# Performance work log

Measured on AMD Instinct MI355X. Metric: run time of the kernel, lower is better.

Reference implementation:

```python
import jax, jax.numpy as jnp
import numpy as np

NUM_CLASSES = 5
SMOOTH = 1e-5


def setup_inputs() -> dict:
    key = jax.random.key(0)
    k1, k2, k3 = jax.random.split(key, 3)
    B, C, X, Y, Z = 2, NUM_CLASSES, 128, 128, 128
    net_output = jax.random.normal(k1, (B, C, X, Y, Z), dtype=jnp.float32)
    target = jax.random.randint(k2, (B, 1, X, Y, Z), 0, C, dtype=jnp.int64)
    dist = jax.random.uniform(k3, (B, 1, X, Y, Z), dtype=jnp.float32)
    return {"net_output": net_output, "target": target, "dist": dist}


def reference(net_output, target, dist):
    # --- Distance-map penalized multi-class Dice ---
    p = jax.nn.softmax(net_output, axis=1)  # (B,C,X,Y,Z)
    gt = target[:, 0]  # (B,X,Y,Z)
    classes = jnp.arange(NUM_CLASSES)[None, :, None, None, None]
    y_onehot = (gt[:, None] == classes).astype(p.dtype)  # (B,C,X,Y,Z)
    # per-class, per-batch sums over spatial dims
    tp = jnp.sum(p * y_onehot * dist, axis=(2, 3, 4))  # (B,C), dist broadcasts over C
    denom = jnp.sum(p, axis=(2, 3, 4)) + jnp.sum(y_onehot, axis=(2, 3, 4))  # (B,C)
    dc = (2.0 * tp + SMOOTH) / (denom + SMOOTH)  # (B,C)
    # sum over classes of batch-mean, divided by num_classes == overall mean
    dpdc_loss = -jnp.mean(dc)
    # --- Cross entropy (mean over all voxels), target squeezed to class idx ---
    logp = jax.nn.log_softmax(net_output, axis=1)  # (B,C,X,Y,Z)
    nll = -jnp.take_along_axis(logp, target, axis=1)  # (B,1,X,Y,Z)
    ce_loss = jnp.mean(nll)
    # aggregate == 'sum', weight_ce = weight_dice = 1
    return ce_loss + dpdc_loss
```

## Files before the change

### kernel.cpp

```cpp
#include <hip/hip_runtime.h>

#define NC 5
#define NB 2
#define SPATIAL (128*128*128)
#define WTILE_VOX 256
#define BTILE_VOX 1024
#define NSTEPS (SPATIAL/BTILE_VOX)
#define GX 256
#define TPB (NSTEPS/GX)
#define SMOOTHF 1e-5f

#define WBUF 8192


__device__ __forceinline__ void async16(const void* g, void* l) {
    __builtin_amdgcn_global_load_lds(
        (const __attribute__((address_space(1))) void*)g,
        (__attribute__((address_space(3))) void*)l, 16, 0, 0);
}

__global__ __launch_bounds__(256) void dpdc_main(
    const float* __restrict__ net, const void* __restrict__ targ,
    const float* __restrict__ dist, float* __restrict__ slots)
{
    __shared__ __align__(16) char lds[2][4][WBUF];
    const int tid = threadIdx.x, wave = tid >> 6, lane = tid & 63;
    const int b = blockIdx.y;

    const unsigned long long tv = ((const unsigned long long*)targ)[lane];
    const int t64 = (__ballot(tv >= 5ull) == 0ull);

    const char* netb  = (const char*)net  + (size_t)b * NC * SPATIAL * 4;
    const char* distb = (const char*)dist + (size_t)b * SPATIAL * 4;
    const char* targb = (const char*)targ + (size_t)b * SPATIAL * (t64 ? 8 : 4);

    const size_t vb0 = (size_t)blockIdx.x * TPB * BTILE_VOX
                     + (size_t)wave * WTILE_VOX;

    auto stage = [&](int k, int bf) {
        char* base = &lds[bf][wave][0];
        const size_t vb = vb0 + (size_t)k * BTILE_VOX;
        const char* ns = netb + vb * 4 + lane * 16;
        #pragma unroll
        for (int c = 0; c < NC; ++c)
            async16(ns + (size_t)c * SPATIAL * 4, base + c * 1024 + lane * 16);
        async16(distb + vb * 4 + lane * 16, base + 5120 + lane * 16);
        if (t64) {
            const char* ts = targb + vb * 8 + lane * 16;
            async16(ts,        base + 6144 + lane * 16);
            async16(ts + 1024, base + 7168 + lane * 16);
        } else {
            const char* ts = targb + vb * 4 + lane * 16;
            async16(ts, base + 6144 + lane * 16);
            async16(ts, base + 7168 + lane * 16);
        }
    };

    float tp[NC], sp[NC];
    #pragma unroll
    for (int c = 0; c < NC; ++c) { tp[c] = 0.f; sp[c] = 0.f; }
    unsigned cntp = 0u;
    float nll = 0.f;

    stage(0, 0);

    #pragma unroll 1
    for (int k = 0; k < TPB; ++k) {
        if (k + 1 < TPB) {
            stage(k + 1, (k + 1) & 1);
            asm volatile("s_waitcnt vmcnt(8)" ::: "memory");
        } else {
            asm volatile("s_waitcnt vmcnt(0)" ::: "memory");
        }
        __builtin_amdgcn_sched_barrier(0);

        const char* base = &lds[k & 1][wave][0];
        float4 l[NC];
        #pragma unroll
        for (int c = 0; c < NC; ++c)
            l[c] = *(const float4*)(base + c * 1024 + lane * 16);
        float4 dd = *(const float4*)(base + 5120 + lane * 16);
        int tt[4];
        if (t64) {
            ulonglong2 a = *(const ulonglong2*)(base + 6144 + lane * 32);
            ulonglong2 q = *(const ulonglong2*)(base + 6144 + lane * 32 + 16);
            tt[0] = (int)a.x; tt[1] = (int)a.y;
            tt[2] = (int)q.x; tt[3] = (int)q.y;
        } else {
            int4 a = *(const int4*)(base + 6144 + lane * 16);
            tt[0] = a.x; tt[1] = a.y; tt[2] = a.z; tt[3] = a.w;
        }
        const float* dv = (const float*)&dd;
        #pragma unroll
        for (int j = 0; j < 4; ++j) {
            float lc[NC];
            #pragma unroll
            for (int c = 0; c < NC; ++c) lc[c] = ((const float*)&l[c])[j];
            float e[NC];
            float s = 0.f;
            #pragma unroll
            for (int c = 0; c < NC; ++c) { e[c] = __expf(lc[c]); s += e[c]; }
            float inv = 1.0f / s;
            int t = tt[j];
            float lsel = lc[4];
            #pragma unroll
            for (int c = 0; c < 4; ++c) lsel = (t == c) ? lc[c] : lsel;
            float pd = dv[j] * inv;
            #pragma unroll
            for (int c = 0; c < NC; ++c) {
                float p = e[c] * inv;
                sp[c] += p;
                tp[c] += (t == c) ? e[c] * pd : 0.f;
            }
            cntp += 1u << (6 * t);
            nll += __logf(s) - lsel;
        }
        asm volatile("s_waitcnt lgkmcnt(0)" ::: "memory");
        __builtin_amdgcn_sched_barrier(0);
    }

    __shared__ float red[4][16];
    float vals[16];
    #pragma unroll
    for (int c = 0; c < NC; ++c) {
        vals[c] = tp[c]; vals[5 + c] = sp[c];
        vals[10 + c] = (float)((cntp >> (6 * c)) & 63u);
    }
    vals[15] = nll;
    #pragma unroll
    for (int k = 0; k < 16; ++k) {
        float v = vals[k];
        #pragma unroll
        for (int off = 32; off > 0; off >>= 1) v += __shfl_down(v, off, 64);
        if (lane == 0) red[wave][k] = v;
    }
    __syncthreads();
    if (tid < 16) {
        float v = red[0][tid] + red[1][tid] + red[2][tid] + red[3][tid];
        slots[((size_t)b * GX + blockIdx.x) * 16 + tid] = v;
    }
}

__global__ __launch_bounds__(1024) void finalize(const float* __restrict__ slots,
                                                 float* __restrict__ out) {
    __shared__ float part[1024];
    __shared__ float tot[32];
    const int j = threadIdx.x;
    const int p = j & 31;
    const int b = p >> 4, k = p & 15;
    float s = 0.f;
    for (int slot = j >> 5; slot < GX; slot += 32)
        s += slots[((size_t)b * GX + slot) * 16 + k];
    part[j] = s;
    __syncthreads();
    if (j < 32) {
        float t = 0.f;
        #pragma unroll
        for (int m = 0; m < 32; ++m) t += part[j + 32 * m];
        tot[j] = t;
    }
    __syncthreads();
    if (j == 0) {
        float dcsum = 0.f;
        for (int bb = 0; bb < NB; ++bb)
            for (int c = 0; c < NC; ++c) {
                float tpv = tot[bb * 16 + c];
                float spv = tot[bb * 16 + 5 + c];
                float cv  = tot[bb * 16 + 10 + c];
                dcsum += (2.f * tpv + SMOOTHF) / (spv + cv + SMOOTHF);
            }
        float ce = (tot[15] + tot[31]) / (float)((size_t)NB * SPATIAL);
        out[0] = ce - dcsum / (float)(NB * NC);
    }
}

extern "C" void kernel_launch(void* const* d_in, const int* in_sizes, int n_in,
                              void* d_out, int out_size, void* d_ws, size_t ws_size,
                              hipStream_t stream) {
    const float* net  = (const float*)d_in[0];
    const void*  targ = d_in[1];
    const float* dist = (const float*)d_in[2];
    float* slots = (float*)d_ws;

    dim3 grid(GX, NB);
    dpdc_main<<<grid, 256, 0, stream>>>(net, targ, dist, slots);
    finalize<<<1, 1024, 0, stream>>>(slots, (float*)d_out);
}
```

Before: 32.43 us.

## Fuse finalize into main kernel via last-block atomic counter; template target width

Removes the separate finalize kernel launch: each block publishes its partial sums with atomics, bumps a global done counter, and the last block to arrive performs the final reduction and writes the loss. The target-width branch is also made a compile-time template, so the int32 path issues one target load per stage instead of a duplicated one and waits with a matching vmcnt. It relies on the workspace counter being zero or 0xAA-filled at start and being reset by the last block. Atomic reads in the tail add some latency to the final block.

New measurement: 33.21 us. 1.02x slower.

```diff
diff --git a/kernel.cpp b/kernel.cpp
--- a/kernel.cpp
+++ b/kernel.cpp
@@ -8,9 +8,10 @@
 #define NSTEPS (SPATIAL/BTILE_VOX)
 #define GX 256
 #define TPB (NSTEPS/GX)
+#define TOTAL_BLOCKS (GX*NB)
 #define SMOOTHF 1e-5f
-
 #define WBUF 8192
+
 
 
 __device__ __forceinline__ void async16(const void* g, void* l) {
@@ -19,24 +20,12 @@
         (__attribute__((address_space(3))) void*)l, 16, 0, 0);
 }
 
-__global__ __launch_bounds__(256) void dpdc_main(
-    const float* __restrict__ net, const void* __restrict__ targ,
-    const float* __restrict__ dist, float* __restrict__ slots)
+template<bool T64>
+__device__ __forceinline__ void pipeline(
+    const char* netb, const char* targb, const char* distb, size_t vb0,
+    int wave, int lane, char (*lds)[4][WBUF],
+    float* tp, float* sp, unsigned& cntp, float& nll)
 {
-    __shared__ __align__(16) char lds[2][4][WBUF];
-    const int tid = threadIdx.x, wave = tid >> 6, lane = tid & 63;
-    const int b = blockIdx.y;
-
-    const unsigned long long tv = ((const unsigned long long*)targ)[lane];
-    const int t64 = (__ballot(tv >= 5ull) == 0ull);
-
-    const char* netb  = (const char*)net  + (size_t)b * NC * SPATIAL * 4;
-    const char* distb = (const char*)dist + (size_t)b * SPATIAL * 4;
-    const char* targb = (const char*)targ + (size_t)b * SPATIAL * (t64 ? 8 : 4);
-
-    const size_t vb0 = (size_t)blockIdx.x * TPB * BTILE_VOX
-                     + (size_t)wave * WTILE_VOX;
-
     auto stage = [&](int k, int bf) {
         char* base = &lds[bf][wave][0];
         const size_t vb = vb0 + (size_t)k * BTILE_VOX;
@@ -45,22 +34,14 @@
         for (int c = 0; c < NC; ++c)
             async16(ns + (size_t)c * SPATIAL * 4, base + c * 1024 + lane * 16);
         async16(distb + vb * 4 + lane * 16, base + 5120 + lane * 16);
-        if (t64) {
+        if constexpr (T64) {
             const char* ts = targb + vb * 8 + lane * 16;
             async16(ts,        base + 6144 + lane * 16);
             async16(ts + 1024, base + 7168 + lane * 16);
         } else {
-            const char* ts = targb + vb * 4 + lane * 16;
-            async16(ts, base + 6144 + lane * 16);
-            async16(ts, base + 7168 + lane * 16);
+            async16(targb + vb * 4 + lane * 16, base + 6144 + lane * 16);
         }
     };
-
-    float tp[NC], sp[NC];
-    #pragma unroll
-    for (int c = 0; c < NC; ++c) { tp[c] = 0.f; sp[c] = 0.f; }
-    unsigned cntp = 0u;
-    float nll = 0.f;
 
     stage(0, 0);
 
@@ -68,7 +49,10 @@
     for (int k = 0; k < TPB; ++k) {
         if (k + 1 < TPB) {
             stage(k + 1, (k + 1) & 1);
-            asm volatile("s_waitcnt vmcnt(8)" ::: "memory");
+            if constexpr (T64)
+                asm volatile("s_waitcnt vmcnt(8)" ::: "memory");
+            else
+                asm volatile("s_waitcnt vmcnt(7)" ::: "memory");
         } else {
             asm volatile("s_waitcnt vmcnt(0)" ::: "memory");
         }
@@ -81,7 +65,7 @@
             l[c] = *(const float4*)(base + c * 1024 + lane * 16);
         float4 dd = *(const float4*)(base + 5120 + lane * 16);
         int tt[4];
-        if (t64) {
+        if constexpr (T64) {
             ulonglong2 a = *(const ulonglong2*)(base + 6144 + lane * 32);
             ulonglong2 q = *(const ulonglong2*)(base + 6144 + lane * 32 + 16);
             tt[0] = (int)a.x; tt[1] = (int)a.y;
@@ -118,6 +102,37 @@
         asm volatile("s_waitcnt lgkmcnt(0)" ::: "memory");
         __builtin_amdgcn_sched_barrier(0);
     }
+}
+
+__global__ __launch_bounds__(256) void dpdc_main(
+    const float* __restrict__ net, const void* __restrict__ targ,
+    const float* __restrict__ dist, float* __restrict__ slots,
+    unsigned* __restrict__ done, float* __restrict__ out)
+{
+    __shared__ __align__(16) char lds[2][4][WBUF];
+    const int tid = threadIdx.x, wave = tid >> 6, lane = tid & 63;
+    const int b = blockIdx.y;
+
+    const unsigned long long tv = ((const unsigned long long*)targ)[lane];
+    const int t64 = (__ballot(tv >= 5ull) == 0ull);
+
+    const char* netb  = (const char*)net  + (size_t)b * NC * SPATIAL * 4;
+    const char* distb = (const char*)dist + (size_t)b * SPATIAL * 4;
+    const char* targb = (const char*)targ + (size_t)b * SPATIAL * (t64 ? 8 : 4);
+
+    const size_t vb0 = (size_t)blockIdx.x * TPB * BTILE_VOX
+                     + (size_t)wave * WTILE_VOX;
+
+    float tp[NC], sp[NC];
+    #pragma unroll
+    for (int c = 0; c < NC; ++c) { tp[c] = 0.f; sp[c] = 0.f; }
+    unsigned cntp = 0u;
+    float nll = 0.f;
+
+    if (t64) pipeline<true >(netb, targb, distb, vb0, wave, lane, lds,
+                             tp, sp, cntp, nll);
+    else     pipeline<false>(netb, targb, distb, vb0, wave, lane, lds,
+                             tp, sp, cntp, nll);
 
     __shared__ float red[4][16];
     float vals[16];
@@ -135,38 +150,58 @@
         if (lane == 0) red[wave][k] = v;
     }
     __syncthreads();
+
+    const int slot = b * GX + blockIdx.x;
     if (tid < 16) {
         float v = red[0][tid] + red[1][tid] + red[2][tid] + red[3][tid];
-        slots[((size_t)b * GX + blockIdx.x) * 16 + tid] = v;
-    }
-}
-
-__global__ __launch_bounds__(1024) void finalize(const float* __restrict__ slots,
-                                                 float* __restrict__ out) {
-    __shared__ float part[1024];
+        float old = __hip_atomic_exchange(&slots[slot * 16 + tid], v,
+                                          __ATOMIC_RELAXED,
+                                          __HIP_MEMORY_SCOPE_AGENT);
+        asm volatile("" :: "v"(old));
+    }
+    asm volatile("s_waitcnt vmcnt(0)" ::: "memory");
+    __builtin_amdgcn_sched_barrier(0);
+    __shared__ int is_last;
+    if (tid == 0) {
+        unsigned old = __hip_atomic_fetch_add(done, 1u, __ATOMIC_RELAXED,
+                                              __HIP_MEMORY_SCOPE_AGENT);
+        unsigned n1 = old + 1u;
+        is_last = (n1 == (unsigned)TOTAL_BLOCKS) ||
+                  (n1 == 0xAAAAAAAAu + (unsigned)TOTAL_BLOCKS);
+    }
+    __syncthreads();
+    if (!is_last) return;
+
+    if (tid == 0) {
+        unsigned o = __hip_atomic_exchange(done, 0u, __ATOMIC_RELAXED,
+                                           __HIP_MEMORY_SCOPE_AGENT);
+        asm volatile("" :: "v"(o));
+    }
+    __shared__ float part[256];
     __shared__ float tot[32];
-    const int j = threadIdx.x;
-    const int p = j & 31;
-    const int b = p >> 4, k = p & 15;
+    const int p = tid & 31, bb = p >> 4, kk = p & 15, chunk = tid >> 5;
     float s = 0.f;
-    for (int slot = j >> 5; slot < GX; slot += 32)
-        s += slots[((size_t)b * GX + slot) * 16 + k];
-    part[j] = s;
-    __syncthreads();
-    if (j < 32) {
+    #pragma unroll 4
+    for (int sl = chunk; sl < GX; sl += 8)
+        s += __hip_atomic_fetch_add(&slots[(bb * GX + sl) * 16 + kk], 0.0f,
+                                    __ATOMIC_RELAXED,
+                                    __HIP_MEMORY_SCOPE_AGENT);
+    part[tid] = s;
+    __syncthreads();
+    if (tid < 32) {
         float t = 0.f;
         #pragma unroll
-        for (int m = 0; m < 32; ++m) t += part[j + 32 * m];
-        tot[j] = t;
-    }
-    __syncthreads();
-    if (j == 0) {
+        for (int m = 0; m < 8; ++m) t += part[tid + 32 * m];
+        tot[tid] = t;
+    }
+    __syncthreads();
+    if (tid == 0) {
         float dcsum = 0.f;
-        for (int bb = 0; bb < NB; ++bb)
+        for (int b2 = 0; b2 < NB; ++b2)
             for (int c = 0; c < NC; ++c) {
-                float tpv = tot[bb * 16 + c];
-                float spv = tot[bb * 16 + 5 + c];
-                float cv  = tot[bb * 16 + 10 + c];
+                float tpv = tot[b2 * 16 + c];
+                float spv = tot[b2 * 16 + 5 + c];
+                float cv  = tot[b2 * 16 + 10 + c];
                 dcsum += (2.f * tpv + SMOOTHF) / (spv + cv + SMOOTHF);
             }
         float ce = (tot[15] + tot[31]) / (float)((size_t)NB * SPATIAL);
@@ -180,9 +215,10 @@
     const float* net  = (const float*)d_in[0];
     const void*  targ = d_in[1];
     const float* dist = (const float*)d_in[2];
-    float* slots = (float*)d_ws;
+    float* slots   = (float*)d_ws;
+    unsigned* done = (unsigned*)((char*)d_ws + TOTAL_BLOCKS * 16 * sizeof(float));
 
     dim3 grid(GX, NB);
-    dpdc_main<<<grid, 256, 0, stream>>>(net, targ, dist, slots);
-    finalize<<<1, 1024, 0, stream>>>(slots, (float*)d_out);
-}
+    dpdc_main<<<grid, 256, 0, stream>>>(net, targ, dist, slots, done,
+                                        (float*)d_out);
+}
```
